# Kernel tuning notes

Hardware: AMD Instinct MI355X
Metric: run time of the kernel (lower is better)

The kernel has to match this reference:

```python
import jax, jax.numpy as jnp
import numpy as np

B, C, H, W = 16, 512, 32, 32
G = 32            # GroupNorm groups (hard-coded in Normalize)
EPS = 1e-6
TEXT = 180        # text_ch
F = H * W         # in_features, asserted H*W == in_features


def setup_inputs() -> dict:
    key = jax.random.key(0)
    ks = jax.random.split(key, 10)
    s = 0.02
    return {
        "x": jax.random.normal(ks[0], (B, C, H, W), dtype=jnp.float32),
        "condition": jax.random.normal(ks[1], (B, TEXT), dtype=jnp.float32),
        "gamma": jnp.ones((C,), dtype=jnp.float32),
        "beta": jnp.zeros((C,), dtype=jnp.float32),
        "wq": jax.random.normal(ks[2], (C, C), dtype=jnp.float32) * s,   # 1x1 conv [out,in]
        "bq": jax.random.normal(ks[3], (C,), dtype=jnp.float32) * s,
        "wk": jax.random.normal(ks[4], (F, TEXT), dtype=jnp.float32) * s,  # Linear(text_ch -> in_features)
        "bk": jax.random.normal(ks[5], (F,), dtype=jnp.float32) * s,
        "wv": jax.random.normal(ks[6], (F, TEXT), dtype=jnp.float32) * s,
        "bv": jax.random.normal(ks[7], (F,), dtype=jnp.float32) * s,
        "wo": jax.random.normal(ks[8], (C, C), dtype=jnp.float32) * s,   # proj_out 1x1 conv
        "bo": jax.random.normal(ks[9], (C,), dtype=jnp.float32) * s,
    }


def _group_norm(x, gamma, beta):
    b, c, h, w = x.shape
    xg = x.reshape(b, G, c // G, h, w)
    mu = xg.mean(axis=(2, 3, 4), keepdims=True)
    var = xg.var(axis=(2, 3, 4), keepdims=True)
    xn = ((xg - mu) * jax.lax.rsqrt(var + EPS)).reshape(b, c, h, w)
    return xn * gamma[None, :, None, None] + beta[None, :, None, None]


def reference(x, condition, gamma, beta, wq, bq, wk, bk, wv, bv, wo, bo):
    h_ = _group_norm(x, gamma, beta)                       # [B,C,H,W]
    # q: 1x1 conv
    q = jnp.einsum('bchw,oc->bohw', h_, wq) + bq[None, :, None, None]
    # condition.reshape(B,1,-1).repeat(1,C,1)
    cond = jnp.broadcast_to(condition[:, None, :], (B, C, TEXT))  # [B,C,T]
    k = jnp.einsum('bct,ft->bcf', cond, wk) + bk           # [B,C,F]
    v = jnp.einsum('bct,ft->bcf', cond, wv) + bv           # [B,C,F]
    q3 = q.reshape(B, C, H * W).transpose(0, 2, 1)         # [B,N,C], N=HW
    scale = C ** (-0.5)
    attn = jax.nn.softmax(jnp.einsum('bnc,bcf->bnf', q3, k) * scale, axis=2)  # [B,N,F]
    h2 = jnp.einsum('bcf,bnf->bcn', v, attn).reshape(B, C, H, W)
    out = jnp.einsum('bchw,oc->bohw', h2, wo) + bo[None, :, None, None]
    return x + out
```

## Files before the change

kernel.cpp:

```cpp
#include <hip/hip_runtime.h>

#define B_   16
#define C_   512
#define N_   1024
#define F_   1024
#define T_   180
#define G_   32

#define WS_MU    0
#define WS_RSIG  512
#define WS_K     1024
#define WS_V     (1024 + 16384)
#define WS_WOS   (1024 + 2*16384)
#define WS_BQS   (WS_WOS + 512)
#define WS_POFF  (WS_BQS + 4)
#define WS_P     36864

__global__ __launch_bounds__(256) void k_prep(
    const float* __restrict__ x, const float* __restrict__ gamma,
    const float* __restrict__ beta, const float* __restrict__ cond,
    const float* __restrict__ wq, const float* __restrict__ bq,
    const float* __restrict__ wk, const float* __restrict__ bk,
    const float* __restrict__ wv, const float* __restrict__ bv,
    const float* __restrict__ wo, float* __restrict__ ws)
{
    const int blk = blockIdx.x;
    const int tid = threadIdx.x;

    if (blk < 512) {
        const int g  = blk & 31;
        const int c0 = g << 4;

        const float4* xv = (const float4*)(x + (size_t)blk * 16384);
        float4 xr[16];
        #pragma unroll
        for (int j = 0; j < 16; ++j) xr[j] = xv[tid + (j << 8)];

        __shared__ float wqpart[16][16];
        {
            const int j  = tid & 15;
            const int oi = tid >> 4;
            const float* wqp = wq + (size_t)oi * C_ + c0 + j;
            float a = 0.f;
            #pragma unroll 8
            for (int k = 0; k < 32; ++k)
                a += wqp[(size_t)(k << 4) * C_];
            wqpart[oi][j] = a;
        }
        __syncthreads();
        __shared__ float wl[16], bwl[16];
        if (tid < 16) {
            float wqs = 0.f;
            #pragma unroll
            for (int k = 0; k < 16; ++k) wqs += wqpart[k][tid];
            const int c = c0 + tid;
            wl[tid]  = gamma[c] * wqs;
            bwl[tid] = beta[c]  * wqs;
        }
        __syncthreads();

        float4 p4 = make_float4(0.f, 0.f, 0.f, 0.f);
        float s = 0.f, sq = 0.f;
        #pragma unroll
        for (int j = 0; j < 16; ++j) {
            float4 p = xr[j];
            s  += (p.x + p.y) + (p.z + p.w);
            sq += p.x * p.x + p.y * p.y + p.z * p.z + p.w * p.w;
            const float wj = wl[j];
            p4.x = fmaf(p.x, wj, p4.x);
            p4.y = fmaf(p.y, wj, p4.y);
            p4.z = fmaf(p.z, wj, p4.z);
            p4.w = fmaf(p.w, wj, p4.w);
        }
        *(float4*)(ws + WS_P + (size_t)blk * 1024 + (tid << 2)) = p4;

        __shared__ float rs[4], rq[4];
        #pragma unroll
        for (int off = 32; off; off >>= 1) {
            s  += __shfl_down(s,  off, 64);
            sq += __shfl_down(sq, off, 64);
        }
        if ((tid & 63) == 0) { rs[tid >> 6] = s; rq[tid >> 6] = sq; }
        __syncthreads();
        if (tid == 0) {
            const float S1 = rs[0] + rs[1] + rs[2] + rs[3];
            const float S2 = rq[0] + rq[1] + rq[2] + rq[3];
            const float mu  = S1 * (1.f / 16384.f);
            const float var = S2 * (1.f / 16384.f) - mu * mu;
            const float rsig = rsqrtf(var + 1e-6f);
            ws[WS_MU   + blk] = mu;
            ws[WS_RSIG + blk] = rsig;
            float sw = 0.f, sbw = 0.f;
            #pragma unroll
            for (int j = 0; j < 16; ++j) { sw += wl[j]; sbw += bwl[j]; }
            ws[WS_POFF + blk] = sbw - mu * rsig * sw;
        }
    } else if (blk < 576) {
        const int idx = blk - 512;
        const int b   = idx >> 2;
        const int f   = ((idx & 3) << 8) + tid;
        __shared__ __align__(16) float condl[T_];
        if (tid < T_) condl[tid] = cond[b * T_ + tid];
        __syncthreads();
        const float4* c4  = (const float4*)condl;
        const float4* wk4 = (const float4*)(wk + (size_t)f * T_);
        const float4* wv4 = (const float4*)(wv + (size_t)f * T_);
        float accK = bk[f];
        float accV = bv[f];
        #pragma unroll 5
        for (int t4 = 0; t4 < 45; ++t4) {
            float4 cf = c4[t4];
            float4 a  = wk4[t4];
            float4 vv = wv4[t4];
            accK = fmaf(cf.x, a.x,  fmaf(cf.y, a.y,  fmaf(cf.z, a.z,  fmaf(cf.w, a.w,  accK))));
            accV = fmaf(cf.x, vv.x, fmaf(cf.y, vv.y, fmaf(cf.z, vv.z, fmaf(cf.w, vv.w, accV))));
        }
        ws[WS_K + b * F_ + f] = accK;
        ws[WS_V + b * F_ + f] = accV;
    } else if (blk < 592) {
        const int o0 = (blk - 576) << 5;
        const int r  = tid >> 3;
        const int j  = tid & 7;
        const float4* row = (const float4*)(wo + (size_t)(o0 + r) * C_);
        float acc = 0.f;
        #pragma unroll
        for (int jj = 0; jj < 16; ++jj) {
            float4 p = row[(jj << 3) + j];
            acc += (p.x + p.y) + (p.z + p.w);
        }
        #pragma unroll
        for (int off = 4; off; off >>= 1) acc += __shfl_down(acc, off, 8);
        if (j == 0) ws[WS_WOS + o0 + r] = acc;
    } else {
        float p = bq[tid] + bq[tid + 256];
        #pragma unroll
        for (int off = 32; off; off >>= 1) p += __shfl_down(p, off, 64);
        __shared__ float rb[4];
        if ((tid & 63) == 0) rb[tid >> 6] = p;
        __syncthreads();
        if (tid == 0) ws[WS_BQS] = rb[0] + rb[1] + rb[2] + rb[3];
    }
}

__global__ __launch_bounds__(256) void k_fused(
    const float* __restrict__ x, const float* __restrict__ bo,
    const float* __restrict__ ws, float* __restrict__ out)
{
    const int b   = blockIdx.x >> 5;
    const int n0  = (blockIdx.x & 31) << 5;
    const int tid = threadIdx.x;

    __shared__ __align__(16) float KV[2 * F_];
    __shared__ float rsigl[32];
    __shared__ float part[8][32];
    __shared__ float pse[8][32], psv[8][32];
    __shared__ float Sl[32], Al[32];
    __shared__ float redmx[4], redmn[4];
    __shared__ float opw;

    if (tid < 32) rsigl[tid] = ws[WS_RSIG + (b << 5) + tid];
    float op = (tid < 32) ? ws[WS_POFF + (b << 5) + tid] : 0.f;

    const float* Kg = ws + WS_K + b * F_;
    const float* Vg = ws + WS_V + b * F_;
    float mx = -1e30f, mn = 1e30f;
    float2* KV2 = (float2*)KV;
    #pragma unroll
    for (int i = tid; i < F_; i += 256) {
        float kv = Kg[i];
        KV2[i] = make_float2(kv, Vg[i]);
        mx = fmaxf(mx, kv);
        mn = fminf(mn, kv);
    }
    #pragma unroll
    for (int off = 32; off; off >>= 1) {
        op += __shfl_down(op, off, 64);
        mx = fmaxf(mx, __shfl_down(mx, off, 64));
        mn = fminf(mn, __shfl_down(mn, off, 64));
    }
    if ((tid & 63) == 0) {
        redmx[tid >> 6] = mx;
        redmn[tid >> 6] = mn;
        if (tid == 0) opw = op + ws[WS_BQS];
    }
    __syncthreads();
    const float offset = opw;
    const float maxK = fmaxf(fmaxf(redmx[0], redmx[1]), fmaxf(redmx[2], redmx[3]));
    const float minK = fminf(fminf(redmn[0], redmn[1]), fminf(redmn[2], redmn[3]));

    const int nl = tid & 31;
    const int gq = tid >> 5;
    {
        const float* Pp = ws + WS_P + ((size_t)((b << 5) + (gq << 2)) << 10) + n0 + nl;
        float acc = 0.f;
        #pragma unroll
        for (int j = 0; j < 4; ++j)
            acc = fmaf(rsigl[(gq << 2) + j], Pp[(size_t)j << 10], acc);
        part[gq][nl] = acc;
    }
    __syncthreads();
    if (tid < 32) {
        float s8 = 0.f;
        #pragma unroll
        for (int j = 0; j < 8; ++j) s8 += part[j][tid];
        Sl[tid] = s8 + offset;
    }
    __syncthreads();

    const float LOG2E = 1.4426950408889634f;
    const float scale = 0.044194173824159216f;
    const float s  = Sl[nl] * scale;
    const float sl = s * LOG2E;
    const float ml = (s >= 0.f ? maxK : minK) * sl;

    float se = 0.f, sv = 0.f;
    const int fq = tid >> 5;
    const int fbase = fq << 7;
    #pragma unroll 8
    for (int fi = 0; fi < 128; ++fi) {
        float2 kv = KV2[fbase + fi];
        float e = exp2f(fmaf(sl, kv.x, -ml));
        se += e;
        sv = fmaf(kv.y, e, sv);
    }
    pse[fq][nl] = se;
    psv[fq][nl] = sv;

    const int col = tid & 7;
    const int row = tid >> 3;
    const float* WOS = ws + WS_WOS;
    float wv_[16], bo_[16];
    #pragma unroll
    for (int p = 0; p < 16; ++p) {
        wv_[p] = WOS[(p << 5) + row];
        bo_[p] = bo[(p << 5) + row];
    }

    __syncthreads();
    if (tid < 32) {
        float den = 0.f, num = 0.f;
        #pragma unroll
        for (int j = 0; j < 8; ++j) { den += pse[j][tid]; num += psv[j][tid]; }
        Al[tid] = num / den;
    }
    __syncthreads();

    float av[4];
    #pragma unroll
    for (int j = 0; j < 4; ++j) av[j] = Al[(col << 2) + j];

    #pragma unroll
    for (int p = 0; p < 16; ++p) {
        const int o = (p << 5) + row;
        const size_t base = (((size_t)(b * C_ + o)) << 10) + n0 + (col << 2);
        float4 xv = *(const float4*)(x + base);
        float4 ov;
        ov.x = xv.x + fmaf(av[0], wv_[p], bo_[p]);
        ov.y = xv.y + fmaf(av[1], wv_[p], bo_[p]);
        ov.z = xv.z + fmaf(av[2], wv_[p], bo_[p]);
        ov.w = xv.w + fmaf(av[3], wv_[p], bo_[p]);
        *(float4*)(out + base) = ov;
    }
}

extern "C" void kernel_launch(void* const* d_in, const int* in_sizes, int n_in,
                              void* d_out, int out_size, void* d_ws, size_t ws_size,
                              hipStream_t stream) {
    const float* x     = (const float*)d_in[0];
    const float* cond  = (const float*)d_in[1];
    const float* gamma = (const float*)d_in[2];
    const float* beta  = (const float*)d_in[3];
    const float* wq    = (const float*)d_in[4];
    const float* bq    = (const float*)d_in[5];
    const float* wk    = (const float*)d_in[6];
    const float* bk    = (const float*)d_in[7];
    const float* wv    = (const float*)d_in[8];
    const float* bv    = (const float*)d_in[9];
    const float* wo    = (const float*)d_in[10];
    const float* bo    = (const float*)d_in[11];
    float* ws  = (float*)d_ws;
    float* out = (float*)d_out;

    hipLaunchKernelGGL(k_prep, dim3(593), dim3(256), 0, stream,
                       x, gamma, beta, cond, wq, bq, wk, bk, wv, bv, wo, ws);
    hipLaunchKernelGGL(k_fused, dim3(512), dim3(256), 0, stream,
                       x, bo, ws, out);
}
```

Baseline: 124.8 us.

## Fuse prep and attention kernels into one cooperative kernel with grid sync

Merges the two launches into a single cooperative kernel of 512 blocks. Each block now does its own share of the K/V projection, wo row sums and group statistics, then waits on a grid-wide barrier before the attention/output phase. This removes the second launch and the tail of the uneven prep grid, and redistributes the K/V and wo work across all blocks. The cost is a grid-sync barrier and a launch-bounds occupancy constraint. The kernel also relies on all 512 blocks being co-resident, which the cooperative launch requires.

```diff
diff --git a/kernel.cpp b/kernel.cpp
--- a/kernel.cpp
+++ b/kernel.cpp
@@ -1,4 +1,7 @@
 #include <hip/hip_runtime.h>
+#include <hip/hip_cooperative_groups.h>
+
+namespace cg = cooperative_groups;
 
 #define B_   16
 #define C_   512
@@ -16,49 +19,108 @@
 #define WS_POFF  (WS_BQS + 4)
 #define WS_P     36864
 
-__global__ __launch_bounds__(256) void k_prep(
+__global__ __launch_bounds__(256, 2) void k_all(
     const float* __restrict__ x, const float* __restrict__ gamma,
     const float* __restrict__ beta, const float* __restrict__ cond,
     const float* __restrict__ wq, const float* __restrict__ bq,
     const float* __restrict__ wk, const float* __restrict__ bk,
     const float* __restrict__ wv, const float* __restrict__ bv,
-    const float* __restrict__ wo, float* __restrict__ ws)
+    const float* __restrict__ wo, const float* __restrict__ bo,
+    float* __restrict__ ws, float* __restrict__ out)
 {
     const int blk = blockIdx.x;
     const int tid = threadIdx.x;
-
-    if (blk < 512) {
-        const int g  = blk & 31;
-        const int c0 = g << 4;
-
-        const float4* xv = (const float4*)(x + (size_t)blk * 16384);
-        float4 xr[16];
-        #pragma unroll
-        for (int j = 0; j < 16; ++j) xr[j] = xv[tid + (j << 8)];
-
-        __shared__ float wqpart[16][16];
-        {
-            const int j  = tid & 15;
-            const int oi = tid >> 4;
-            const float* wqp = wq + (size_t)oi * C_ + c0 + j;
-            float a = 0.f;
-            #pragma unroll 8
-            for (int k = 0; k < 32; ++k)
-                a += wqp[(size_t)(k << 4) * C_];
-            wqpart[oi][j] = a;
-        }
-        __syncthreads();
-        __shared__ float wl[16], bwl[16];
-        if (tid < 16) {
-            float wqs = 0.f;
-            #pragma unroll
-            for (int k = 0; k < 16; ++k) wqs += wqpart[k][tid];
-            const int c = c0 + tid;
-            wl[tid]  = gamma[c] * wqs;
-            bwl[tid] = beta[c]  * wqs;
-        }
-        __syncthreads();
-
+    const int b   = blk >> 5;
+    const int g   = blk & 31;
+
+    __shared__ __align__(16) float condl[184];
+    __shared__ float wqpart[16][16];
+    __shared__ float wl[16], bwl[16];
+    __shared__ float rs[4], rq[4];
+    __shared__ __align__(16) float KV[2 * F_];
+    __shared__ float rsigl[32];
+    __shared__ float part[8][32];
+    __shared__ float pse[8][32], psv[8][32];
+    __shared__ float Sl[32], Al[32];
+    __shared__ float redmx[4], redmn[4];
+    __shared__ float opw;
+
+    const float4* xv = (const float4*)(x + (size_t)blk * 16384);
+    float4 xr[16];
+    #pragma unroll
+    for (int j = 0; j < 16; ++j) xr[j] = xv[tid + (j << 8)];
+
+    if (tid < T_) condl[tid] = cond[b * T_ + tid];
+
+    {
+        const int j  = tid & 15;
+        const int oi = tid >> 4;
+        const float* wqp = wq + (size_t)oi * C_ + (g << 4) + j;
+        float a = 0.f;
+        #pragma unroll 8
+        for (int k = 0; k < 32; ++k)
+            a += wqp[(size_t)(k << 4) * C_];
+        wqpart[oi][j] = a;
+    }
+    __syncthreads();
+
+    {
+        const int r = tid >> 3;
+        const int j = tid & 7;
+        const int f = (g << 5) + r;
+        const float4* c4  = (const float4*)condl;
+        const float4* wk4 = (const float4*)(wk + (size_t)f * T_);
+        const float4* wv4 = (const float4*)(wv + (size_t)f * T_);
+        float aK = 0.f, aV = 0.f;
+        for (int t4 = j; t4 < 45; t4 += 8) {
+            float4 cf = c4[t4];
+            float4 a  = wk4[t4];
+            float4 vv = wv4[t4];
+            aK = fmaf(cf.x, a.x,  fmaf(cf.y, a.y,  fmaf(cf.z, a.z,  fmaf(cf.w, a.w,  aK))));
+            aV = fmaf(cf.x, vv.x, fmaf(cf.y, vv.y, fmaf(cf.z, vv.z, fmaf(cf.w, vv.w, aV))));
+        }
+        #pragma unroll
+        for (int off = 4; off; off >>= 1) {
+            aK += __shfl_down(aK, off, 8);
+            aV += __shfl_down(aV, off, 8);
+        }
+        if (j == 0) {
+            ws[WS_K + b * F_ + f] = aK + bk[f];
+            ws[WS_V + b * F_ + f] = aV + bv[f];
+        }
+    }
+
+    if (tid < 64) {
+        const float4* row = (const float4*)(wo + (size_t)blk * C_);
+        float4 p0 = row[tid];
+        float4 p1 = row[tid + 64];
+        float a = ((p0.x + p0.y) + (p0.z + p0.w)) + ((p1.x + p1.y) + (p1.z + p1.w));
+        #pragma unroll
+        for (int off = 32; off; off >>= 1) a += __shfl_down(a, off, 64);
+        if (tid == 0) ws[WS_WOS + blk] = a;
+    }
+
+    if (blk == 0 && tid >= 64 && tid < 128) {
+        const int l = tid - 64;
+        float p = 0.f;
+        #pragma unroll
+        for (int k = 0; k < 8; ++k) p += bq[l + (k << 6)];
+        #pragma unroll
+        for (int off = 32; off; off >>= 1) p += __shfl_down(p, off, 64);
+        if (l == 0) ws[WS_BQS] = p;
+    }
+
+    if (tid < 16) {
+        float wqs = 0.f;
+        #pragma unroll
+        for (int k = 0; k < 16; ++k) wqs += wqpart[k][tid];
+        const int c = (g << 4) + tid;
+        wl[tid]  = gamma[c] * wqs;
+        bwl[tid] = beta[c]  * wqs;
+    }
+    __syncthreads();
+
+    {
         float4 p4 = make_float4(0.f, 0.f, 0.f, 0.f);
         float s = 0.f, sq = 0.f;
         #pragma unroll
@@ -74,7 +136,6 @@
         }
         *(float4*)(ws + WS_P + (size_t)blk * 1024 + (tid << 2)) = p4;
 
-        __shared__ float rs[4], rq[4];
         #pragma unroll
         for (int off = 32; off; off >>= 1) {
             s  += __shfl_down(s,  off, 64);
@@ -95,68 +156,12 @@
             for (int j = 0; j < 16; ++j) { sw += wl[j]; sbw += bwl[j]; }
             ws[WS_POFF + blk] = sbw - mu * rsig * sw;
         }
-    } else if (blk < 576) {
-        const int idx = blk - 512;
-        const int b   = idx >> 2;
-        const int f   = ((idx & 3) << 8) + tid;
-        __shared__ __align__(16) float condl[T_];
-        if (tid < T_) condl[tid] = cond[b * T_ + tid];
-        __syncthreads();
-        const float4* c4  = (const float4*)condl;
-        const float4* wk4 = (const float4*)(wk + (size_t)f * T_);
-        const float4* wv4 = (const float4*)(wv + (size_t)f * T_);
-        float accK = bk[f];
-        float accV = bv[f];
-        #pragma unroll 5
-        for (int t4 = 0; t4 < 45; ++t4) {
-            float4 cf = c4[t4];
-            float4 a  = wk4[t4];
-            float4 vv = wv4[t4];
-            accK = fmaf(cf.x, a.x,  fmaf(cf.y, a.y,  fmaf(cf.z, a.z,  fmaf(cf.w, a.w,  accK))));
-            accV = fmaf(cf.x, vv.x, fmaf(cf.y, vv.y, fmaf(cf.z, vv.z, fmaf(cf.w, vv.w, accV))));
-        }
-        ws[WS_K + b * F_ + f] = accK;
-        ws[WS_V + b * F_ + f] = accV;
-    } else if (blk < 592) {
-        const int o0 = (blk - 576) << 5;
-        const int r  = tid >> 3;
-        const int j  = tid & 7;
-        const float4* row = (const float4*)(wo + (size_t)(o0 + r) * C_);
-        float acc = 0.f;
-        #pragma unroll
-        for (int jj = 0; jj < 16; ++jj) {
-            float4 p = row[(jj << 3) + j];
-            acc += (p.x + p.y) + (p.z + p.w);
-        }
-        #pragma unroll
-        for (int off = 4; off; off >>= 1) acc += __shfl_down(acc, off, 8);
-        if (j == 0) ws[WS_WOS + o0 + r] = acc;
-    } else {
-        float p = bq[tid] + bq[tid + 256];
-        #pragma unroll
-        for (int off = 32; off; off >>= 1) p += __shfl_down(p, off, 64);
-        __shared__ float rb[4];
-        if ((tid & 63) == 0) rb[tid >> 6] = p;
-        __syncthreads();
-        if (tid == 0) ws[WS_BQS] = rb[0] + rb[1] + rb[2] + rb[3];
-    }
-}
-
-__global__ __launch_bounds__(256) void k_fused(
-    const float* __restrict__ x, const float* __restrict__ bo,
-    const float* __restrict__ ws, float* __restrict__ out)
-{
-    const int b   = blockIdx.x >> 5;
-    const int n0  = (blockIdx.x & 31) << 5;
-    const int tid = threadIdx.x;
-
-    __shared__ __align__(16) float KV[2 * F_];
-    __shared__ float rsigl[32];
-    __shared__ float part[8][32];
-    __shared__ float pse[8][32], psv[8][32];
-    __shared__ float Sl[32], Al[32];
-    __shared__ float redmx[4], redmn[4];
-    __shared__ float opw;
+    }
+
+    __threadfence();
+    cg::this_grid().sync();
+
+    const int n0 = g << 5;
 
     if (tid < 32) rsigl[tid] = ws[WS_RSIG + (b << 5) + tid];
     float op = (tid < 32) ? ws[WS_POFF + (b << 5) + tid] : 0.f;
@@ -253,12 +258,12 @@
     for (int p = 0; p < 16; ++p) {
         const int o = (p << 5) + row;
         const size_t base = (((size_t)(b * C_ + o)) << 10) + n0 + (col << 2);
-        float4 xv = *(const float4*)(x + base);
+        float4 x4 = *(const float4*)(x + base);
         float4 ov;
-        ov.x = xv.x + fmaf(av[0], wv_[p], bo_[p]);
-        ov.y = xv.y + fmaf(av[1], wv_[p], bo_[p]);
-        ov.z = xv.z + fmaf(av[2], wv_[p], bo_[p]);
-        ov.w = xv.w + fmaf(av[3], wv_[p], bo_[p]);
+        ov.x = x4.x + fmaf(av[0], wv_[p], bo_[p]);
+        ov.y = x4.y + fmaf(av[1], wv_[p], bo_[p]);
+        ov.z = x4.z + fmaf(av[2], wv_[p], bo_[p]);
+        ov.w = x4.w + fmaf(av[3], wv_[p], bo_[p]);
         *(float4*)(out + base) = ov;
     }
 }
@@ -281,8 +286,11 @@
     float* ws  = (float*)d_ws;
     float* out = (float*)d_out;
 
-    hipLaunchKernelGGL(k_prep, dim3(593), dim3(256), 0, stream,
-                       x, gamma, beta, cond, wq, bq, wk, bk, wv, bv, wo, ws);
-    hipLaunchKernelGGL(k_fused, dim3(512), dim3(256), 0, stream,
-                       x, bo, ws, out);
+    void* args[] = {
+        (void*)&x, (void*)&gamma, (void*)&beta, (void*)&cond,
+        (void*)&wq, (void*)&bq, (void*)&wk, (void*)&bk,
+        (void*)&wv, (void*)&bv, (void*)&wo, (void*)&bo,
+        (void*)&ws, (void*)&out
+    };
+    hipLaunchCooperativeKernel((void*)k_all, dim3(512), dim3(256), args, 0, stream);
 }
```

Result: slower. 207.8 us (+66.5%).
